# Kernel optimization log

Hardware: AMD Instinct MI355X
Metric: run time of the kernel (lower is better)

The kernel has to match this reference:

```python
import jax, jax.numpy as jnp
import numpy as np

B, T, H = 128, 2048, 128


def setup_inputs() -> dict:
    key = jax.random.key(0)
    ks = jax.random.split(key, 8)
    stdv = 1.0 / np.sqrt(H)
    u = lambda k: jax.random.uniform(k, (H, H), jnp.float32, -stdv, stdv)
    return {
        "x": jax.random.normal(ks[0], (B, T, H), jnp.float32),
        "lengths": jax.random.randint(ks[1], (B,), 1, T + 1),
        "W_z": u(ks[2]), "U_z": u(ks[3]), "b_z": jnp.zeros((H,), jnp.float32),
        "W_r": u(ks[4]), "U_r": u(ks[5]), "b_r": jnp.zeros((H,), jnp.float32),
        "W_h": u(ks[6]), "U_h": u(ks[7]), "b_h": jnp.zeros((H,), jnp.float32),
    }


def reference(x, lengths, W_z, U_z, b_z, W_r, U_r, b_r, W_h, U_h, b_h):
    # Input-side projections batched over all timesteps as single GEMMs.
    # torch `W @ x_t` with x_t (B,H,1) == einsum('ij,bj->bi', W, x_t)
    xz = jnp.einsum('btj,ij->bti', x, W_z) + b_z  # [B,T,H]
    xr = jnp.einsum('btj,ij->bti', x, W_r) + b_r
    xh = jnp.einsum('btj,ij->bti', x, W_h) + b_h

    def step(h, ins):
        xz_t, xr_t, xh_t = ins
        z = jax.nn.sigmoid(xz_t + h @ U_z.T)
        r = jax.nn.sigmoid(xr_t + h @ U_r.T)
        h_cand = jnp.tanh(xh_t + (r * h) @ U_h.T)
        h = (1.0 - z) * h + z * h_cand
        return h, h

    h0 = jnp.zeros((x.shape[0], H), x.dtype)
    xs = (jnp.swapaxes(xz, 0, 1), jnp.swapaxes(xr, 0, 1), jnp.swapaxes(xh, 0, 1))
    _, hs = jax.lax.scan(step, h0, xs)  # [T,B,H]
    h_out = jnp.swapaxes(hs, 0, 1)      # [B,T,H]

    # pack_padded_sequence drops positions beyond each sequence length;
    # emulate by zero-masking the padded positions.
    mask = (jnp.arange(x.shape[1])[None, :] < lengths[:, None])[:, :, None]
    return h_out * mask.astype(h_out.dtype)
```

## Files before the change

### kernel.cpp

```cpp
#include <hip/hip_runtime.h>


#define T_LEN 2048
#define H_DIM 128

typedef __attribute__((ext_vector_type(8))) __bf16 bf16x8;
typedef __attribute__((ext_vector_type(4))) float f32x4;

#define BARRIER() asm volatile("s_waitcnt lgkmcnt(0)\n\ts_barrier" ::: "memory")

__device__ __forceinline__ unsigned short f2bf_bits(float f){
  __bf16 b = (__bf16)f;
  return __builtin_bit_cast(unsigned short, b);
}
__device__ __forceinline__ float bf2f(unsigned short s){
  unsigned int u = ((unsigned int)s) << 16;
  return __builtin_bit_cast(float, u);
}
__device__ __forceinline__ unsigned int pack_bf16_rne(float lo, float hi){
  return (unsigned int)f2bf_bits(lo) | (((unsigned int)f2bf_bits(hi)) << 16);
}
__device__ __forceinline__ float sigm(float x){
  float e = __builtin_amdgcn_exp2f(-1.4426950408889634f * x);
  return __builtin_amdgcn_rcpf(1.0f + e);
}
__device__ __forceinline__ float tanh_fast(float x){
  float e = __builtin_amdgcn_exp2f(2.8853900817779268f * x);
  return 1.0f - 2.0f * __builtin_amdgcn_rcpf(e + 1.0f);
}
__device__ __forceinline__ float dpp_xor1(float x){
  int r = __builtin_amdgcn_update_dpp(0, __builtin_bit_cast(int, x),
                                      0xB1, 0xF, 0xF, true);
  return __builtin_bit_cast(float, r);
}


__device__ __forceinline__ void stage_mat128(const float* __restrict__ src,
                                             __bf16 (*dst)[136], int tid){
  #pragma unroll
  for (int rep = 0; rep < 8; ++rep){
    int fi = rep * 2048 + tid * 4;
    float4 v = *reinterpret_cast<const float4*>(src + fi);
    int m = fi >> 7;
    int k = fi & 127;
    unsigned long long pk =
        (unsigned long long)f2bf_bits(v.x)
      | ((unsigned long long)f2bf_bits(v.y) << 16)
      | ((unsigned long long)f2bf_bits(v.z) << 32)
      | ((unsigned long long)f2bf_bits(v.w) << 48);
    *reinterpret_cast<unsigned long long*>(&dst[m][k]) = pk;
  }
}

__global__ __launch_bounds__(512, 2) void gru_proj(
    const float* __restrict__ x,
    const float* __restrict__ Wz, const float* __restrict__ Wr, const float* __restrict__ Wh,
    const float* __restrict__ bz, const float* __restrict__ br, const float* __restrict__ bh,
    unsigned int* __restrict__ out_zr, unsigned short* __restrict__ out_h)
{
  __shared__ __bf16 xs[128][136];
  __shared__ __bf16 wsh[3][128][136];

  const int tid = threadIdx.x;
  const long Mbase = (long)blockIdx.x * 128;

  stage_mat128(x + Mbase * H_DIM, xs, tid);
  stage_mat128(Wz, wsh[0], tid);
  stage_mat128(Wr, wsh[1], tid);
  stage_mat128(Wh, wsh[2], tid);
  __syncthreads();

  const int w  = tid >> 6, l = tid & 63;
  const int ml = l & 15;
  const int kl = (l >> 4) * 8;
  const int n  = w * 16 + ml;

  bf16x8 bfr[3][4];
  #pragma unroll
  for (int g = 0; g < 3; ++g)
    #pragma unroll
    for (int kk = 0; kk < 4; ++kk)
      bfr[g][kk] = *reinterpret_cast<const bf16x8*>(&wsh[g][n][kk * 32 + kl]);

  const float bzv = bz[n], brv = br[n], bhv = bh[n];

  f32x4 acc[8][3];
  #pragma unroll
  for (int mt = 0; mt < 8; ++mt)
    #pragma unroll
    for (int g = 0; g < 3; ++g)
      acc[mt][g] = (f32x4){0.f, 0.f, 0.f, 0.f};

  #pragma unroll
  for (int mt = 0; mt < 8; ++mt){
    #pragma unroll
    for (int kk = 0; kk < 4; ++kk){
      bf16x8 a = *reinterpret_cast<const bf16x8*>(&xs[mt * 16 + ml][kk * 32 + kl]);
      acc[mt][0] = __builtin_amdgcn_mfma_f32_16x16x32_bf16(a, bfr[0][kk], acc[mt][0], 0, 0, 0);
      acc[mt][1] = __builtin_amdgcn_mfma_f32_16x16x32_bf16(a, bfr[1][kk], acc[mt][1], 0, 0, 0);
      acc[mt][2] = __builtin_amdgcn_mfma_f32_16x16x32_bf16(a, bfr[2][kk], acc[mt][2], 0, 0, 0);
    }
  }

  #pragma unroll
  for (int mt = 0; mt < 8; ++mt){
    #pragma unroll
    for (int p = 0; p < 4; ++p){
      long row = Mbase + mt * 16 + (l >> 4) * 4 + p;
      float vz = acc[mt][0][p] + bzv;
      float vr = acc[mt][1][p] + brv;
      float vh = acc[mt][2][p] + bhv;
      unsigned int word = (unsigned int)f2bf_bits(vz)
                        | (((unsigned int)f2bf_bits(vr)) << 16);
      out_zr[row * H_DIM + n] = word;
      out_h [row * H_DIM + n] = f2bf_bits(vh);
    }
  }
}


__device__ __forceinline__ bf16x8 ld_u_frag(const float* p){
  float4 a = *reinterpret_cast<const float4*>(p);
  float4 b = *reinterpret_cast<const float4*>(p + 4);
  bf16x8 r;
  r[0]=(__bf16)a.x; r[1]=(__bf16)a.y; r[2]=(__bf16)a.z; r[3]=(__bf16)a.w;
  r[4]=(__bf16)b.x; r[5]=(__bf16)b.y; r[6]=(__bf16)b.z; r[7]=(__bf16)b.w;
  return r;
}

#define MFMA(A, B, C) __builtin_amdgcn_mfma_f32_16x16x32_bf16(A, B, C, 0, 0, 0)

__device__ __forceinline__ void gru_step8(
    int t, int ub, int g8, int l, int w,
    const bf16x8* ufz, const bf16x8* ufr, const bf16x8* ufh,
    __bf16* hx, __bf16* rhx,
    const unsigned int* xzr, const unsigned short* xh, float* out,
    unsigned int& zrw, unsigned short& xhw, float& h_own)
{
  const f32x4 zero = (f32x4){0.f, 0.f, 0.f, 0.f};
  const int tp = (t + 4 < T_LEN) ? t + 4 : T_LEN - 1;
  const bool wr = ((l & 1) == 0) & (l < 16);

  bf16x8 a0 = *reinterpret_cast<const bf16x8*>(&hx[      g8 * 8]);
  bf16x8 a1 = *reinterpret_cast<const bf16x8*>(&hx[32  + g8 * 8]);
  bf16x8 a2 = *reinterpret_cast<const bf16x8*>(&hx[64  + g8 * 8]);
  bf16x8 a3 = *reinterpret_cast<const bf16x8*>(&hx[96  + g8 * 8]);
  f32x4 r0 = MFMA(a0, ufr[0], zero);
  f32x4 r1 = MFMA(a1, ufr[1], zero);
  f32x4 r2 = MFMA(a2, ufr[2], zero);
  f32x4 r3 = MFMA(a3, ufr[3], zero);

  float xzv = bf2f((unsigned short)(zrw & 0xffffu));
  float xrv = bf2f((unsigned short)(zrw >> 16));
  float xhv = bf2f(xhw);
  zrw = xzr[ub + tp * H_DIM];
  xhw = xh [ub + tp * H_DIM];

  float rg = sigm(xrv + ((r0[0] + r1[0]) + (r2[0] + r3[0])));
  float rh  = rg * h_own;
  float rhn = dpp_xor1(rh);
  if (wr)
    *reinterpret_cast<unsigned int*>(&rhx[w * 16 + (l & 14)]) = pack_bf16_rne(rh, rhn);
  BARRIER();

  bf16x8 b0 = *reinterpret_cast<const bf16x8*>(&rhx[      g8 * 8]);
  bf16x8 b1 = *reinterpret_cast<const bf16x8*>(&rhx[32  + g8 * 8]);
  bf16x8 b2 = *reinterpret_cast<const bf16x8*>(&rhx[64  + g8 * 8]);
  bf16x8 b3 = *reinterpret_cast<const bf16x8*>(&rhx[96  + g8 * 8]);
  f32x4 z0 = MFMA(a0, ufz[0], zero);
  f32x4 z1 = MFMA(a1, ufz[1], zero);
  f32x4 z2 = MFMA(a2, ufz[2], zero);
  f32x4 z3 = MFMA(a3, ufz[3], zero);
  f32x4 h0 = MFMA(b0, ufh[0], zero);
  f32x4 h1 = MFMA(b1, ufh[1], zero);
  f32x4 h2 = MFMA(b2, ufh[2], zero);
  f32x4 h3 = MFMA(b3, ufh[3], zero);

  float zg = sigm(xzv + ((z0[0] + z1[0]) + (z2[0] + z3[0])));
  float hc = tanh_fast(xhv + ((h0[0] + h1[0]) + (h2[0] + h3[0])));
  float hn = fmaf(zg, hc - h_own, h_own);
  h_own = hn;
  float hnn = dpp_xor1(hn);
  if (wr)
    *reinterpret_cast<unsigned int*>(&hx[w * 16 + (l & 14)]) = pack_bf16_rne(hn, hnn);
  if (l < 16)
    out[ub + t * H_DIM] = hn;
  BARRIER();
}

__global__ __launch_bounds__(512, 1) void gru_rec8p(
    const float* __restrict__ Uz, const float* __restrict__ Ur, const float* __restrict__ Uh,
    const int* __restrict__ lengths,
    const unsigned int* xzr,
    const unsigned short* __restrict__ xh,
    float* out)
{
  __shared__ __align__(16) __bf16 hx[H_DIM];
  __shared__ __align__(16) __bf16 rhx[H_DIM];

  const int tid = threadIdx.x;
  const int w = tid >> 6, l = tid & 63;
  const int g8 = l >> 4;
  const int u  = w * 16 + (l & 15);
  const int b  = blockIdx.x;
  const int len = lengths[b];

  bf16x8 ufz[4], ufr[4], ufh[4];
  #pragma unroll
  for (int kk = 0; kk < 4; ++kk){
    const int ko = kk * 32 + g8 * 8;
    ufz[kk] = ld_u_frag(Uz + u * H_DIM + ko);
    ufr[kk] = ld_u_frag(Ur + u * H_DIM + ko);
    ufh[kk] = ld_u_frag(Uh + u * H_DIM + ko);
  }

  if (tid < 64) reinterpret_cast<unsigned int*>(hx)[tid] = 0u;
  float h_own = 0.f;
  __syncthreads();

  const int ub = b * (T_LEN * H_DIM) + u;

  unsigned int  zrA = xzr[ub];
  unsigned int  zrB = xzr[ub + 1 * H_DIM];
  unsigned int  zrC = xzr[ub + 2 * H_DIM];
  unsigned int  zrD = xzr[ub + 3 * H_DIM];
  unsigned short xhA = xh[ub];
  unsigned short xhB = xh[ub + 1 * H_DIM];
  unsigned short xhC = xh[ub + 2 * H_DIM];
  unsigned short xhD = xh[ub + 3 * H_DIM];

  int t = 0;
  for (; t + 3 < len; t += 4){
    gru_step8(t,   ub, g8, l, w, ufz, ufr, ufh, hx, rhx, xzr, xh, out, zrA, xhA, h_own);
    gru_step8(t+1, ub, g8, l, w, ufz, ufr, ufh, hx, rhx, xzr, xh, out, zrB, xhB, h_own);
    gru_step8(t+2, ub, g8, l, w, ufz, ufr, ufh, hx, rhx, xzr, xh, out, zrC, xhC, h_own);
    gru_step8(t+3, ub, g8, l, w, ufz, ufr, ufh, hx, rhx, xzr, xh, out, zrD, xhD, h_own);
  }
  if (t < len)
    gru_step8(t,   ub, g8, l, w, ufz, ufr, ufh, hx, rhx, xzr, xh, out, zrA, xhA, h_own);
  if (t + 1 < len)
    gru_step8(t+1, ub, g8, l, w, ufz, ufr, ufh, hx, rhx, xzr, xh, out, zrB, xhB, h_own);
  if (t + 2 < len)
    gru_step8(t+2, ub, g8, l, w, ufz, ufr, ufh, hx, rhx, xzr, xh, out, zrC, xhC, h_own);

  const long base = (long)b * (T_LEN * H_DIM);
  for (long i = (long)len * H_DIM + tid * 4; i < (long)T_LEN * H_DIM; i += 512 * 4){
    *reinterpret_cast<float4*>(out + base + i) = make_float4(0.f, 0.f, 0.f, 0.f);
  }
}

extern "C" void kernel_launch(void* const* d_in, const int* in_sizes, int n_in,
                              void* d_out, int out_size, void* d_ws, size_t ws_size,
                              hipStream_t stream){
  const float* x       = (const float*)d_in[0];
  const int*   lengths = (const int*)  d_in[1];
  const float* Wz = (const float*)d_in[2];
  const float* Uz = (const float*)d_in[3];
  const float* bz = (const float*)d_in[4];
  const float* Wr = (const float*)d_in[5];
  const float* Ur = (const float*)d_in[6];
  const float* br = (const float*)d_in[7];
  const float* Wh = (const float*)d_in[8];
  const float* Uh = (const float*)d_in[9];
  const float* bh = (const float*)d_in[10];

  unsigned int*   zr    = (unsigned int*)d_out;
  unsigned short* xhbuf = (unsigned short*)d_ws;

  gru_proj<<<dim3(2048), dim3(512), 0, stream>>>(x, Wz, Wr, Wh, bz, br, bh, zr, xhbuf);
  gru_rec8p<<<dim3(128), dim3(512), 0, stream>>>(Uz, Ur, Uh, lengths, zr, xhbuf, (float*)d_out);
}
```

Measured before the change: 1.084 ms.

## Fold activation exp2 scales into weights, simplify LDS writes, deepen prefetch

Pre-multiplies the input projections and the recurrent U matrices by the sigmoid/tanh exp2 constants, which removes a multiply from the serial recurrence's critical path. Replaces the DPP-paired packed bf16 LDS stores with direct per-lane 16-bit stores. Raises the prefetch distance and unroll from 4 to 6 timesteps and moves the xh load later in the step. Scaling before bf16 rounding slightly changes numerics, and the single-element LDS stores may conflict more.

```diff
diff --git a/kernel.cpp b/kernel.cpp
--- a/kernel.cpp
+++ b/kernel.cpp
@@ -8,6 +8,9 @@
 typedef __attribute__((ext_vector_type(4))) float f32x4;
 
 #define BARRIER() asm volatile("s_waitcnt lgkmcnt(0)\n\ts_barrier" ::: "memory")
+
+#define KNEG -1.4426950408889634f
+#define KPOS  2.8853900817779268f
 
 __device__ __forceinline__ unsigned short f2bf_bits(float f){
   __bf16 b = (__bf16)f;
@@ -17,21 +20,12 @@
   unsigned int u = ((unsigned int)s) << 16;
   return __builtin_bit_cast(float, u);
 }
-__device__ __forceinline__ unsigned int pack_bf16_rne(float lo, float hi){
-  return (unsigned int)f2bf_bits(lo) | (((unsigned int)f2bf_bits(hi)) << 16);
-}
-__device__ __forceinline__ float sigm(float x){
-  float e = __builtin_amdgcn_exp2f(-1.4426950408889634f * x);
-  return __builtin_amdgcn_rcpf(1.0f + e);
-}
-__device__ __forceinline__ float tanh_fast(float x){
-  float e = __builtin_amdgcn_exp2f(2.8853900817779268f * x);
-  return 1.0f - 2.0f * __builtin_amdgcn_rcpf(e + 1.0f);
-}
-__device__ __forceinline__ float dpp_xor1(float x){
-  int r = __builtin_amdgcn_update_dpp(0, __builtin_bit_cast(int, x),
-                                      0xB1, 0xF, 0xF, true);
-  return __builtin_bit_cast(float, r);
+__device__ __forceinline__ float sigm_pre(float x){
+  return __builtin_amdgcn_rcpf(1.0f + __builtin_amdgcn_exp2f(x));
+}
+__device__ __forceinline__ float tanh_pre(float y){
+  float t = __builtin_amdgcn_rcpf(__builtin_amdgcn_exp2f(y) + 1.0f);
+  return fmaf(-2.0f, t, 1.0f);
 }
 
 
@@ -107,9 +101,9 @@
     #pragma unroll
     for (int p = 0; p < 4; ++p){
       long row = Mbase + mt * 16 + (l >> 4) * 4 + p;
-      float vz = acc[mt][0][p] + bzv;
-      float vr = acc[mt][1][p] + brv;
-      float vh = acc[mt][2][p] + bhv;
+      float vz = (acc[mt][0][p] + bzv) * KNEG;
+      float vr = (acc[mt][1][p] + brv) * KNEG;
+      float vh = (acc[mt][2][p] + bhv) * KPOS;
       unsigned int word = (unsigned int)f2bf_bits(vz)
                         | (((unsigned int)f2bf_bits(vr)) << 16);
       out_zr[row * H_DIM + n] = word;
@@ -119,12 +113,12 @@
 }
 
 
-__device__ __forceinline__ bf16x8 ld_u_frag(const float* p){
+__device__ __forceinline__ bf16x8 ld_u_frag_s(const float* p, float s){
   float4 a = *reinterpret_cast<const float4*>(p);
   float4 b = *reinterpret_cast<const float4*>(p + 4);
   bf16x8 r;
-  r[0]=(__bf16)a.x; r[1]=(__bf16)a.y; r[2]=(__bf16)a.z; r[3]=(__bf16)a.w;
-  r[4]=(__bf16)b.x; r[5]=(__bf16)b.y; r[6]=(__bf16)b.z; r[7]=(__bf16)b.w;
+  r[0]=(__bf16)(a.x*s); r[1]=(__bf16)(a.y*s); r[2]=(__bf16)(a.z*s); r[3]=(__bf16)(a.w*s);
+  r[4]=(__bf16)(b.x*s); r[5]=(__bf16)(b.y*s); r[6]=(__bf16)(b.z*s); r[7]=(__bf16)(b.w*s);
   return r;
 }
 
@@ -138,8 +132,9 @@
     unsigned int& zrw, unsigned short& xhw, float& h_own)
 {
   const f32x4 zero = (f32x4){0.f, 0.f, 0.f, 0.f};
-  const int tp = (t + 4 < T_LEN) ? t + 4 : T_LEN - 1;
-  const bool wr = ((l & 1) == 0) & (l < 16);
+  const int tp = (t + 6 < T_LEN) ? t + 6 : T_LEN - 1;
+  const int u  = w * 16 + (l & 15);
+  const bool own = (l < 16);
 
   bf16x8 a0 = *reinterpret_cast<const bf16x8*>(&hx[      g8 * 8]);
   bf16x8 a1 = *reinterpret_cast<const bf16x8*>(&hx[32  + g8 * 8]);
@@ -153,14 +148,12 @@
   float xzv = bf2f((unsigned short)(zrw & 0xffffu));
   float xrv = bf2f((unsigned short)(zrw >> 16));
   float xhv = bf2f(xhw);
+
+  float rg = sigm_pre(xrv + ((r0[0] + r1[0]) + (r2[0] + r3[0])));
+  float rh = rg * h_own;
+  if (own)
+    rhx[u] = (__bf16)rh;
   zrw = xzr[ub + tp * H_DIM];
-  xhw = xh [ub + tp * H_DIM];
-
-  float rg = sigm(xrv + ((r0[0] + r1[0]) + (r2[0] + r3[0])));
-  float rh  = rg * h_own;
-  float rhn = dpp_xor1(rh);
-  if (wr)
-    *reinterpret_cast<unsigned int*>(&rhx[w * 16 + (l & 14)]) = pack_bf16_rne(rh, rhn);
   BARRIER();
 
   bf16x8 b0 = *reinterpret_cast<const bf16x8*>(&rhx[      g8 * 8]);
@@ -176,19 +169,19 @@
   f32x4 h2 = MFMA(b2, ufh[2], zero);
   f32x4 h3 = MFMA(b3, ufh[3], zero);
 
-  float zg = sigm(xzv + ((z0[0] + z1[0]) + (z2[0] + z3[0])));
-  float hc = tanh_fast(xhv + ((h0[0] + h1[0]) + (h2[0] + h3[0])));
+  float zg = sigm_pre(xzv + ((z0[0] + z1[0]) + (z2[0] + z3[0])));
+  float hc = tanh_pre(xhv + ((h0[0] + h1[0]) + (h2[0] + h3[0])));
   float hn = fmaf(zg, hc - h_own, h_own);
   h_own = hn;
-  float hnn = dpp_xor1(hn);
-  if (wr)
-    *reinterpret_cast<unsigned int*>(&hx[w * 16 + (l & 14)]) = pack_bf16_rne(hn, hnn);
-  if (l < 16)
+  if (own){
+    hx[u] = (__bf16)hn;
     out[ub + t * H_DIM] = hn;
+  }
+  xhw = xh[ub + tp * H_DIM];
   BARRIER();
 }
 
-__global__ __launch_bounds__(512, 1) void gru_rec8p(
+__global__ __launch_bounds__(512, 1) void gru_rec8q(
     const float* __restrict__ Uz, const float* __restrict__ Ur, const float* __restrict__ Uh,
     const int* __restrict__ lengths,
     const unsigned int* xzr,
@@ -209,9 +202,9 @@
   #pragma unroll
   for (int kk = 0; kk < 4; ++kk){
     const int ko = kk * 32 + g8 * 8;
-    ufz[kk] = ld_u_frag(Uz + u * H_DIM + ko);
-    ufr[kk] = ld_u_frag(Ur + u * H_DIM + ko);
-    ufh[kk] = ld_u_frag(Uh + u * H_DIM + ko);
+    ufz[kk] = ld_u_frag_s(Uz + u * H_DIM + ko, KNEG);
+    ufr[kk] = ld_u_frag_s(Ur + u * H_DIM + ko, KNEG);
+    ufh[kk] = ld_u_frag_s(Uh + u * H_DIM + ko, KPOS);
   }
 
   if (tid < 64) reinterpret_cast<unsigned int*>(hx)[tid] = 0u;
@@ -224,17 +217,23 @@
   unsigned int  zrB = xzr[ub + 1 * H_DIM];
   unsigned int  zrC = xzr[ub + 2 * H_DIM];
   unsigned int  zrD = xzr[ub + 3 * H_DIM];
+  unsigned int  zrE = xzr[ub + 4 * H_DIM];
+  unsigned int  zrF = xzr[ub + 5 * H_DIM];
   unsigned short xhA = xh[ub];
   unsigned short xhB = xh[ub + 1 * H_DIM];
   unsigned short xhC = xh[ub + 2 * H_DIM];
   unsigned short xhD = xh[ub + 3 * H_DIM];
+  unsigned short xhE = xh[ub + 4 * H_DIM];
+  unsigned short xhF = xh[ub + 5 * H_DIM];
 
   int t = 0;
-  for (; t + 3 < len; t += 4){
+  for (; t + 5 < len; t += 6){
     gru_step8(t,   ub, g8, l, w, ufz, ufr, ufh, hx, rhx, xzr, xh, out, zrA, xhA, h_own);
     gru_step8(t+1, ub, g8, l, w, ufz, ufr, ufh, hx, rhx, xzr, xh, out, zrB, xhB, h_own);
     gru_step8(t+2, ub, g8, l, w, ufz, ufr, ufh, hx, rhx, xzr, xh, out, zrC, xhC, h_own);
     gru_step8(t+3, ub, g8, l, w, ufz, ufr, ufh, hx, rhx, xzr, xh, out, zrD, xhD, h_own);
+    gru_step8(t+4, ub, g8, l, w, ufz, ufr, ufh, hx, rhx, xzr, xh, out, zrE, xhE, h_own);
+    gru_step8(t+5, ub, g8, l, w, ufz, ufr, ufh, hx, rhx, xzr, xh, out, zrF, xhF, h_own);
   }
   if (t < len)
     gru_step8(t,   ub, g8, l, w, ufz, ufr, ufh, hx, rhx, xzr, xh, out, zrA, xhA, h_own);
@@ -242,6 +241,10 @@
     gru_step8(t+1, ub, g8, l, w, ufz, ufr, ufh, hx, rhx, xzr, xh, out, zrB, xhB, h_own);
   if (t + 2 < len)
     gru_step8(t+2, ub, g8, l, w, ufz, ufr, ufh, hx, rhx, xzr, xh, out, zrC, xhC, h_own);
+  if (t + 3 < len)
+    gru_step8(t+3, ub, g8, l, w, ufz, ufr, ufh, hx, rhx, xzr, xh, out, zrD, xhD, h_own);
+  if (t + 4 < len)
+    gru_step8(t+4, ub, g8, l, w, ufz, ufr, ufh, hx, rhx, xzr, xh, out, zrE, xhE, h_own);
 
   const long base = (long)b * (T_LEN * H_DIM);
   for (long i = (long)len * H_DIM + tid * 4; i < (long)T_LEN * H_DIM; i += 512 * 4){
@@ -268,5 +271,5 @@
   unsigned short* xhbuf = (unsigned short*)d_ws;
 
   gru_proj<<<dim3(2048), dim3(512), 0, stream>>>(x, Wz, Wr, Wh, bz, br, bh, zr, xhbuf);
-  gru_rec8p<<<dim3(128), dim3(512), 0, stream>>>(Uz, Ur, Uh, lengths, zr, xhbuf, (float*)d_out);
-}
+  gru_rec8q<<<dim3(128), dim3(512), 0, stream>>>(Uz, Ur, Uh, lengths, zr, xhbuf, (float*)d_out);
+}
```

Measured after the change: 970.6 us (median of 2 runs). 1.12x faster.
